# Kernel tuning notes

Measured on AMD Instinct MI355X. Metric: run time of the kernel, lower is better.

The kernel has to match this reference:

```python
import jax, jax.numpy as jnp
import numpy as np

N = 100000      # nodes
E = 1600000     # edges
IN = 128        # in_channels
HID = 32        # hidden_channels
HEADS = 4
G = 256         # number of graphs in the batch
NEG_SLOPE = 0.2


def setup_inputs() -> dict:
    key = jax.random.key(0)
    ks = jax.random.split(key, 20)
    s = 0.1
    d = {
        'x': jax.random.normal(ks[0], (N, IN), jnp.float32),
        'edge_index': jax.random.randint(ks[1], (2, E), 0, N, dtype=jnp.int64),
        'batch': jnp.sort(jax.random.randint(ks[2], (N,), 0, G, dtype=jnp.int64)),
        # conv1: IN -> HID per head, HEADS heads, concat
        'W1': jax.random.normal(ks[3], (IN, HEADS * HID), jnp.float32) * s,
        'a_src1': jax.random.normal(ks[4], (HEADS, HID), jnp.float32) * s,
        'a_dst1': jax.random.normal(ks[5], (HEADS, HID), jnp.float32) * s,
        'b1': jnp.zeros((HEADS * HID,), jnp.float32),
        # conv2: HEADS*HID -> HID per head, HEADS heads, concat
        'W2': jax.random.normal(ks[6], (HEADS * HID, HEADS * HID), jnp.float32) * s,
        'a_src2': jax.random.normal(ks[7], (HEADS, HID), jnp.float32) * s,
        'a_dst2': jax.random.normal(ks[8], (HEADS, HID), jnp.float32) * s,
        'b2': jnp.zeros((HEADS * HID,), jnp.float32),
        # conv3: HEADS*HID -> HID, 1 head, no concat (mean over heads is identity)
        'W3': jax.random.normal(ks[9], (HEADS * HID, HID), jnp.float32) * s,
        'a_src3': jax.random.normal(ks[10], (1, HID), jnp.float32) * s,
        'a_dst3': jax.random.normal(ks[11], (1, HID), jnp.float32) * s,
        'b3': jnp.zeros((HID,), jnp.float32),
        # final readout
        'fc_w': jax.random.normal(ks[12], (HID, 1), jnp.float32) * s,
        'fc_b': jnp.zeros((1,), jnp.float32),
    }
    return d


def _gat_layer(x, src, dst, W, a_s, a_d, b, concat):
    """One PyG-style GATConv: edge attention logits, per-destination softmax, scatter-aggregate."""
    n = x.shape[0]
    H, C = a_s.shape
    h = (x @ W).reshape(n, H, C)                       # [N, H, C]
    asrc = (h * a_s).sum(-1)                           # [N, H]
    adst = (h * a_d).sum(-1)                           # [N, H]
    e = jax.nn.leaky_relu(asrc[src] + adst[dst], NEG_SLOPE)   # [Etot, H]
    m = jax.ops.segment_max(e, dst, num_segments=n)    # per-dst max (self-loops guarantee non-empty)
    ex = jnp.exp(e - m[dst])
    den = jax.ops.segment_sum(ex, dst, num_segments=n)
    alpha = ex / (den[dst] + 1e-16)                    # segment softmax, [Etot, H]
    out = jax.ops.segment_sum(alpha[:, :, None] * h[src], dst, num_segments=n)  # [N, H, C]
    if concat:
        return out.reshape(n, H * C) + b
    return out.mean(axis=1) + b


def reference(x, edge_index, batch, W1, a_src1, a_dst1, b1, W2, a_src2, a_dst2, b2,
              W3, a_src3, a_dst3, b3, fc_w, fc_b):
    n = x.shape[0]
    loops = jnp.arange(n, dtype=edge_index.dtype)      # GATConv adds self-loops by default
    src = jnp.concatenate([edge_index[0], loops])
    dst = jnp.concatenate([edge_index[1], loops])

    h = jax.nn.elu(_gat_layer(x, src, dst, W1, a_src1, a_dst1, b1, True))
    h = jax.nn.elu(_gat_layer(h, src, dst, W2, a_src2, a_dst2, b2, True))
    h = jax.nn.elu(_gat_layer(h, src, dst, W3, a_src3, a_dst3, b3, False))

    counts = jax.ops.segment_sum(jnp.ones((n,), h.dtype), batch, num_segments=G)
    pooled = jax.ops.segment_sum(h, batch, num_segments=G) / jnp.maximum(counts, 1.0)[:, None]
    # dropout p=0.5 is identity in eval mode
    return pooled @ fc_w + fc_b                        # [G, 1]
```

## Files before the change

### kernel.cpp

```cpp
#include <hip/hip_runtime.h>
#include <hip/hip_bf16.h>
#include <math.h>

#define NEG_SLOPE 0.2f
#define CHUNK 6144

typedef short bf16x8 __attribute__((ext_vector_type(8)));
typedef float f32x4  __attribute__((ext_vector_type(4)));

__device__ __forceinline__ float leaky(float x){ return x > 0.f ? x : NEG_SLOPE*x; }
__device__ __forceinline__ float elu(float x){ return x > 0.f ? x : expm1f(x); }

__device__ __forceinline__ ushort f2bf(float f){
  uint u = __float_as_uint(f);
  u += 0x7fffu + ((u >> 16) & 1u);
  return (ushort)(u >> 16);
}
__device__ __forceinline__ uint pk2(float lo, float hi){
  return (uint)f2bf(lo) | ((uint)f2bf(hi) << 16);
}
__device__ __forceinline__ float2 bfpair(uint v){
  return make_float2(__uint_as_float(v << 16), __uint_as_float(v & 0xffff0000u));
}

__global__ __launch_bounds__(256) void k_histA(const int* __restrict__ ei, int E,
                                               int* __restrict__ bucketCount){
  __shared__ int hist[512];
  for (int b = threadIdx.x; b < 512; b += 256) hist[b] = 0;
  __syncthreads();
  int base = blockIdx.x * 2048;
  int cnt = min(2048, E - base);
  for (int i = threadIdx.x; i < cnt; i += 256)
    atomicAdd(&hist[ei[E + base + i] >> 8], 1);
  __syncthreads();
  for (int b = threadIdx.x; b < 512; b += 256)
    if (hist[b]) atomicAdd(&bucketCount[b], hist[b]);
}

__global__ __launch_bounds__(256) void k_scanB(const int* __restrict__ bucketCount, int NB,
                        int* __restrict__ bucketBase, int* __restrict__ gcursor, int E){
  __shared__ int s[512];
  for (int b = threadIdx.x; b < 512; b += 256)
    s[b] = (b < NB) ? bucketCount[b] : 0;
  __syncthreads();
  if (threadIdx.x == 0){
    int run = 0;
    for (int b = 0; b < NB; b++){ int v = s[b]; s[b] = run; run += v; }
  }
  __syncthreads();
  for (int b = threadIdx.x; b < NB; b += 256){
    bucketBase[b] = s[b]; gcursor[b] = s[b];
  }
  if (threadIdx.x == 0) bucketBase[NB] = E;
}

__global__ __launch_bounds__(256) void k_scatA(const int* __restrict__ ei, int E, int NB,
                         int* __restrict__ gcursor, uint* __restrict__ tmp){
  __shared__ uint stageS[CHUNK];
  __shared__ uint stageD[CHUNK];
  __shared__ int hist[512], pre[512], cur[512], gbase[512];
  __shared__ int scanArr[256];
  int tid = threadIdx.x;
  int base = blockIdx.x * CHUNK;
  int cnt = min(CHUNK, E - base);
  for (int b = tid; b < 512; b += 256) hist[b] = 0;
  __syncthreads();
  for (int i = tid; i < cnt; i += 256)
    atomicAdd(&hist[ei[E + base + i] >> 8], 1);
  __syncthreads();
  int a0 = hist[2*tid], a1 = hist[2*tid+1];
  scanArr[tid] = a0 + a1;
  __syncthreads();
  for (int st = 1; st < 256; st <<= 1){
    int v = (tid >= st) ? scanArr[tid - st] : 0;
    __syncthreads();
    scanArr[tid] += v;
    __syncthreads();
  }
  int eb = tid ? scanArr[tid-1] : 0;
  pre[2*tid] = eb;        cur[2*tid] = eb;
  pre[2*tid+1] = eb + a0; cur[2*tid+1] = eb + a0;
  if (2*tid < NB && a0 > 0)   gbase[2*tid]   = atomicAdd(&gcursor[2*tid],   a0);
  if (2*tid+1 < NB && a1 > 0) gbase[2*tid+1] = atomicAdd(&gcursor[2*tid+1], a1);
  __syncthreads();
  for (int i = tid; i < cnt; i += 256){
    int s = ei[base + i];
    int d = ei[E + base + i];
    int lpos = atomicAdd(&cur[d >> 8], 1);
    stageS[lpos] = (uint)s; stageD[lpos] = (uint)d;
  }
  __syncthreads();
  for (int i = tid; i < cnt; i += 256){
    uint d = stageD[i];
    int b = d >> 8;
    tmp[gbase[b] + (i - pre[b])] = (stageS[i] << 8) | (d & 255u);
  }
}

__global__ __launch_bounds__(256) void k_csr(const uint* __restrict__ tmp,
                      const int* __restrict__ bucketBase,
                      int N, int NB, int* __restrict__ offsets, int* __restrict__ csr,
                      int* __restrict__ edst){
  int b = blockIdx.x;
  int nodeBase = b << 8;
  int nNodes = min(256, N - nodeBase);
  int eBeg = bucketBase[b], eEnd = bucketBase[b+1];
  __shared__ int deg[256], cur[256];
  int tid = threadIdx.x;
  deg[tid] = 0;
  __syncthreads();
  for (int e = eBeg + tid; e < eEnd; e += 256)
    atomicAdd(&deg[tmp[e] & 255u], 1);
  __syncthreads();
  cur[tid] = deg[tid];
  __syncthreads();
  for (int st = 1; st < 256; st <<= 1){
    int w = (tid >= st) ? cur[tid - st] : 0;
    __syncthreads();
    cur[tid] += w;
    __syncthreads();
  }
  int excl = tid ? cur[tid-1] : 0;
  __syncthreads();
  cur[tid] = excl;
  if (tid < nNodes) offsets[nodeBase + tid] = eBeg + excl;
  if (b == NB-1 && tid == 0) offsets[N] = eEnd;
  __syncthreads();
  for (int e = eBeg + tid; e < eEnd; e += 256){
    uint u = tmp[e];
    int lpos = atomicAdd(&cur[u & 255u], 1);
    csr[eBeg + lpos] = (int)(u >> 8);
    edst[eBeg + lpos] = nodeBase + (int)(u & 255u);
  }
}

template<int NT>
__global__ __launch_bounds__(256) void k_wrep(const float* __restrict__ W, ushort* __restrict__ Wf){
  int idx = blockIdx.x*256 + threadIdx.x;
  if (idx >= NT*4*64) return;
  int lane = idx & 63;
  int c = (idx >> 6) & 3;
  int t = idx >> 8;
  int col = t*16 + (lane & 15);
  int k0 = c*32 + (lane >> 4)*8;
  uint4 o;
  const float* p0 = W + (size_t)k0*(NT*16) + col;
  o.x = pk2(p0[0],          p0[NT*16]);
  o.y = pk2(p0[2*NT*16],    p0[3*NT*16]);
  o.z = pk2(p0[4*NT*16],    p0[5*NT*16]);
  o.w = pk2(p0[6*NT*16],    p0[7*NT*16]);
  *(uint4*)(Wf + (size_t)idx*8) = o;
}

template<int NT, bool A_F32>
__global__ __launch_bounds__(256) void k_mgemm(const void* __restrict__ Xv,
                     const ushort* __restrict__ Wf, ushort* __restrict__ Y, int n){
  constexpr int M = NT*16;
  int lane = threadIdx.x & 63;
  int l15 = lane & 15, q = lane >> 4;
  int wgid = blockIdx.x*4 + (threadIdx.x >> 6);
  int nchunks = (n + 15) >> 4;
  int stride = gridDim.x*4;

  bf16x8 bw[NT][4];
  #pragma unroll
  for (int t = 0; t < NT; t++)
    #pragma unroll
    for (int c = 0; c < 4; c++)
      bw[t][c] = *(const bf16x8*)(Wf + (size_t)(((t<<2)+c)*64 + lane)*8);

  int chunk = wgid;
  if (chunk >= nchunks) return;

  bf16x8 aCur[4], aNext[4];
  auto loadA = [&](int ck, bf16x8* a){
    int m = ck*16 + l15;
    if (m >= n) m = n - 1;
    if (A_F32){
      const float* X = (const float*)Xv + (size_t)m*128 + q*8;
      #pragma unroll
      for (int c = 0; c < 4; c++){
        float4 u0 = *(const float4*)(X + c*32);
        float4 u1 = *(const float4*)(X + c*32 + 4);
        uint4 pkd;
        pkd.x = pk2(u0.x, u0.y); pkd.y = pk2(u0.z, u0.w);
        pkd.z = pk2(u1.x, u1.y); pkd.w = pk2(u1.z, u1.w);
        union { uint4 u; bf16x8 v; } cv; cv.u = pkd;
        a[c] = cv.v;
      }
    } else {
      const ushort* X = (const ushort*)Xv + (size_t)m*128 + q*8;
      #pragma unroll
      for (int c = 0; c < 4; c++) a[c] = *(const bf16x8*)(X + c*32);
    }
  };

  loadA(chunk, aCur);
  while (true){
    int nx = chunk + stride;
    if (nx < nchunks) loadA(nx, aNext);
    f32x4 acc[NT];
    #pragma unroll
    for (int t = 0; t < NT; t++) acc[t] = (f32x4){0.f,0.f,0.f,0.f};
    #pragma unroll
    for (int c = 0; c < 4; c++)
      #pragma unroll
      for (int t = 0; t < NT; t++)
        acc[t] = __builtin_amdgcn_mfma_f32_16x16x32_bf16(aCur[c], bw[t][c], acc[t], 0, 0, 0);
    int rowb = chunk*16 + q*4;
    #pragma unroll
    for (int t = 0; t < NT; t++)
      #pragma unroll
      for (int r = 0; r < 4; r++){
        int row = rowb + r;
        if (row < n) Y[(size_t)row*M + t*16 + l15] = f2bf(acc[t][r]);
      }
    if (nx >= nchunks) break;
    chunk = nx;
    #pragma unroll
    for (int c = 0; c < 4; c++) aCur[c] = aNext[c];
  }
}

__global__ __launch_bounds__(256) void k_attn(const ushort* __restrict__ Hb, const float* __restrict__ a_s,
                     const float* __restrict__ a_d, float* __restrict__ asrc, float* __restrict__ adst,
                     int n, int H, int M){
  int idx = blockIdx.x*256 + threadIdx.x;
  if (idx >= n*H) return;
  int node = idx / H, h = idx - node*H;
  const uint4* r4 = (const uint4*)(Hb + (size_t)node*M + h*32);
  const float* as = a_s + h*32;
  const float* ad = a_d + h*32;
  float s1 = 0.f, s2 = 0.f;
  #pragma unroll
  for (int i = 0; i < 4; i++){
    uint4 qv = r4[i];
    uint w[4] = {qv.x, qv.y, qv.z, qv.w};
    #pragma unroll
    for (int j = 0; j < 4; j++){
      float2 f = bfpair(w[j]);
      int c = i*8 + j*2;
      s1 += f.x*as[c] + f.y*as[c+1];
      s2 += f.x*ad[c] + f.y*ad[c+1];
    }
  }
  asrc[idx] = s1; adst[idx] = s2;
}

__global__ __launch_bounds__(256) void k_edgew1(const float* __restrict__ asrc,
                    const float* __restrict__ adst, const int* __restrict__ csr,
                    const int* __restrict__ edst, float* __restrict__ ew, int E){
  int e = blockIdx.x*256 + threadIdx.x;
  if (e >= E) return;
  int s = csr[e], d = edst[e];
  ew[e] = __expf(leaky(asrc[s] + adst[d]));
}

template<bool OUT_BF16>
__global__ __launch_bounds__(256) void k_agg128f(const ushort* __restrict__ Hb,
                    const float* __restrict__ asrc, const float* __restrict__ adst,
                    const int* __restrict__ offsets, const int* __restrict__ csr_src,
                    const float* __restrict__ bias, void* __restrict__ Out, int n){
  __shared__ float lwAll[4][256];
  __shared__ int   lsAll[4][64];
  int wv = threadIdx.x >> 6;
  int lane = threadIdx.x & 63;
  float* lw = lwAll[wv];
  int*   ls = lsAll[wv];
  int node = blockIdx.x*4 + wv;
  if (node >= n) return;
  const int up = lane, ch = up*2, h0 = up >> 4;
  const uint* rows = (const uint*)Hb;
  float4 adv = *(const float4*)(adst + (size_t)node*4);
  float adh = adst[(size_t)node*4 + h0];
  float acc0 = 0.f, acc1 = 0.f, den = 0.f;
  {
    float w = __expf(leaky(asrc[(size_t)node*4 + h0] + adh));
    float2 f = bfpair(rows[(size_t)node*64 + up]);
    den += w; acc0 += w*f.x; acc1 += w*f.y;
  }
  int j0 = offsets[node], end = offsets[node+1];
  for (int base = j0; base < end; base += 64){
    int m = min(64, end - base);
    if (lane < m){
      int s = csr_src[base + lane];
      ls[lane] = s;
      float4 a = *(const float4*)(asrc + (size_t)s*4);
      float4 w4;
      w4.x = __expf(leaky(a.x + adv.x));
      w4.y = __expf(leaky(a.y + adv.y));
      w4.z = __expf(leaky(a.z + adv.z));
      w4.w = __expf(leaky(a.w + adv.w));
      *(float4*)(lw + lane*4) = w4;
    }
    int e = 0;
    for (; e + 8 <= m; e += 8){
      int s0=ls[e+0], s1=ls[e+1], s2=ls[e+2], s3=ls[e+3];
      int s4=ls[e+4], s5=ls[e+5], s6=ls[e+6], s7=ls[e+7];
      float w0=lw[(e+0)*4+h0], w1=lw[(e+1)*4+h0], w2=lw[(e+2)*4+h0], w3=lw[(e+3)*4+h0];
      float w4=lw[(e+4)*4+h0], w5=lw[(e+5)*4+h0], w6=lw[(e+6)*4+h0], w7=lw[(e+7)*4+h0];
      uint r0 = rows[(size_t)s0*64 + up];
      uint r1 = rows[(size_t)s1*64 + up];
      uint r2 = rows[(size_t)s2*64 + up];
      uint r3 = rows[(size_t)s3*64 + up];
      uint r4 = rows[(size_t)s4*64 + up];
      uint r5 = rows[(size_t)s5*64 + up];
      uint r6 = rows[(size_t)s6*64 + up];
      uint r7 = rows[(size_t)s7*64 + up];
      float2 f0=bfpair(r0), f1=bfpair(r1), f2=bfpair(r2), f3=bfpair(r3);
      float2 f4=bfpair(r4), f5=bfpair(r5), f6=bfpair(r6), f7=bfpair(r7);
      den  += ((w0+w1)+(w2+w3)) + ((w4+w5)+(w6+w7));
      acc0 += (w0*f0.x + w1*f1.x + w2*f2.x + w3*f3.x)
            + (w4*f4.x + w5*f5.x + w6*f6.x + w7*f7.x);
      acc1 += (w0*f0.y + w1*f1.y + w2*f2.y + w3*f3.y)
            + (w4*f4.y + w5*f5.y + w6*f6.y + w7*f7.y);
    }
    for (; e < m; e++){
      int s = ls[e];
      float w = lw[e*4 + h0];
      float2 f = bfpair(rows[(size_t)s*64 + up]);
      den += w; acc0 += w*f.x; acc1 += w*f.y;
    }
  }
  float inv = 1.f/(den + 1e-16f);
  float ox = elu(acc0*inv + bias[ch]);
  float oy = elu(acc1*inv + bias[ch+1]);
  if (OUT_BF16){
    ((uint*)Out)[(size_t)node*64 + up] = pk2(ox, oy);
  } else {
    *(float2*)((float*)Out + (size_t)node*128 + ch) = make_float2(ox, oy);
  }
}

__global__ __launch_bounds__(256) void k_agg32(const ushort* __restrict__ Hb,
                    const float* __restrict__ asrc, const float* __restrict__ adst,
                    const float* __restrict__ ew,
                    const int* __restrict__ offsets, const int* __restrict__ csr_src,
                    const float* __restrict__ bias, float* __restrict__ Out, int n){
  constexpr int PAIRS = 16;
  int gid = blockIdx.x*256 + threadIdx.x;
  int wave = gid >> 6;
  int lane = threadIdx.x & 63;
  int node = wave*4 + (lane >> 4);
  int up = lane & 15;
  if (node >= n) return;
  const int ch = up*2;
  const uint* rows = (const uint*)Hb;
  float acc0 = 0.f, acc1 = 0.f, den = 0.f;
  {
    float w = __expf(leaky(asrc[node] + adst[node]));
    float2 f = bfpair(rows[(size_t)node*PAIRS + up]);
    den += w; acc0 += w*f.x; acc1 += w*f.y;
  }
  int j = offsets[node], end = offsets[node+1];
  for (; j + 4 <= end; j += 4){
    int s0 = csr_src[j], s1 = csr_src[j+1], s2 = csr_src[j+2], s3 = csr_src[j+3];
    float w0 = ew[j+0], w1 = ew[j+1], w2 = ew[j+2], w3 = ew[j+3];
    uint r0 = rows[(size_t)s0*PAIRS + up];
    uint r1 = rows[(size_t)s1*PAIRS + up];
    uint r2 = rows[(size_t)s2*PAIRS + up];
    uint r3 = rows[(size_t)s3*PAIRS + up];
    float2 f0 = bfpair(r0), f1 = bfpair(r1), f2 = bfpair(r2), f3 = bfpair(r3);
    den  += (w0 + w1) + (w2 + w3);
    acc0 += w0*f0.x + w1*f1.x + w2*f2.x + w3*f3.x;
    acc1 += w0*f0.y + w1*f1.y + w2*f2.y + w3*f3.y;
  }
  for (; j < end; j++){
    int s = csr_src[j];
    float w = ew[j];
    float2 f = bfpair(rows[(size_t)s*PAIRS + up]);
    den += w; acc0 += w*f.x; acc1 += w*f.y;
  }
  float inv = 1.f/(den + 1e-16f);
  float2 o;
  o.x = elu(acc0*inv + bias[ch]);
  o.y = elu(acc1*inv + bias[ch+1]);
  *(float2*)(Out + (size_t)node*32 + ch) = o;
}

__global__ __launch_bounds__(256) void k_bounds(const int* __restrict__ batch, int n, int G,
                                                int* __restrict__ gstart){
  int i = blockIdx.x*256 + threadIdx.x;
  if (i >= n) return;
  int b = batch[i];
  int bp = (i > 0) ? batch[i-1] : -1;
  for (int g = bp + 1; g <= b; g++) gstart[g] = i;
  if (i == n-1){
    for (int g = b + 1; g <= G; g++) gstart[g] = n;
  }
}

__global__ __launch_bounds__(256) void k_pool2(const float* __restrict__ H3,
                     const int* __restrict__ gstart, const float* __restrict__ fcw,
                     const float* __restrict__ fcb, float* __restrict__ out, int G){
  int g = blockIdx.x;
  int s0 = gstart[g], s1 = gstart[g+1];
  int tid = threadIdx.x;
  int c = tid & 31, r = tid >> 5;
  float sum = 0.f;
  for (int i = s0 + r; i < s1; i += 8)
    sum += H3[(size_t)i*32 + c];
  __shared__ float sh[8][32];
  sh[r][c] = sum;
  __syncthreads();
  if (tid < 32){
    float t = 0.f;
    #pragma unroll
    for (int k = 0; k < 8; k++) t += sh[k][tid];
    t *= fcw[tid];
    #pragma unroll
    for (int off = 16; off; off >>= 1) t += __shfl_down(t, off, 32);
    if (tid == 0){
      float cnt = (float)(s1 - s0); if (cnt < 1.f) cnt = 1.f;
      out[g] = t/cnt + fcb[0];
    }
  }
}

extern "C" void kernel_launch(void* const* d_in, const int* in_sizes, int n_in,
                              void* d_out, int out_size, void* d_ws, size_t ws_size,
                              hipStream_t stream){
  const float* x    = (const float*)d_in[0];
  const int*   ei   = (const int*)d_in[1];
  const int*   batch= (const int*)d_in[2];
  const float* W1   = (const float*)d_in[3];
  const float* as1  = (const float*)d_in[4];
  const float* ad1  = (const float*)d_in[5];
  const float* b1   = (const float*)d_in[6];
  const float* W2   = (const float*)d_in[7];
  const float* as2  = (const float*)d_in[8];
  const float* ad2  = (const float*)d_in[9];
  const float* b2   = (const float*)d_in[10];
  const float* W3   = (const float*)d_in[11];
  const float* as3  = (const float*)d_in[12];
  const float* ad3  = (const float*)d_in[13];
  const float* b3   = (const float*)d_in[14];
  const float* fcw  = (const float*)d_in[15];
  const float* fcb  = (const float*)d_in[16];
  float* out = (float*)d_out;

  const int N = in_sizes[0] / 128;
  const int E = in_sizes[1] / 2;
  const int G = out_size;
  const int NB = (N + 255) >> 8;

  char* p = (char*)d_ws;
  auto alloc = [&](size_t bytes) -> void* {
    void* r = (void*)p;
    p += (bytes + 255) & ~(size_t)255;
    return r;
  };
  ushort* bufH   = (ushort*)alloc((size_t)N*128*sizeof(ushort));
  ushort* aggB   = (ushort*)alloc((size_t)N*128*sizeof(ushort));
  float*  bufA32 = (float*)alloc((size_t)N*32*sizeof(float));
  float*  asrc   = (float*)alloc((size_t)N*4*sizeof(float));
  float*  adst   = (float*)alloc((size_t)N*4*sizeof(float));
  float*  ew     = (float*)alloc((size_t)E*sizeof(float));
  int*    offsets= (int*)alloc((size_t)(N+1)*sizeof(int));
  int*    csr    = (int*)alloc((size_t)E*sizeof(int));
  int*    edst   = (int*)alloc((size_t)E*sizeof(int));
  uint*   tmp    = (uint*)alloc((size_t)E*sizeof(uint));
  int*    bCount = (int*)alloc(512*sizeof(int));
  int*    bBase  = (int*)alloc(520*sizeof(int));
  int*    gcursor= (int*)alloc(512*sizeof(int));
  int*    gstart = (int*)alloc((size_t)(G+1)*sizeof(int));
  ushort* Wf1    = (ushort*)alloc(8*4*64*8*sizeof(ushort));
  ushort* Wf2    = (ushort*)alloc(8*4*64*8*sizeof(ushort));
  ushort* Wf3    = (ushort*)alloc(2*4*64*8*sizeof(ushort));

  hipMemsetAsync(bCount, 0, 512*sizeof(int), stream);

  k_wrep<8><<<8, 256, 0, stream>>>(W1, Wf1);
  k_wrep<8><<<8, 256, 0, stream>>>(W2, Wf2);
  k_wrep<2><<<2, 256, 0, stream>>>(W3, Wf3);

  k_histA<<<(E+2047)/2048, 256, 0, stream>>>(ei, E, bCount);
  k_scanB<<<1, 256, 0, stream>>>(bCount, NB, bBase, gcursor, E);
  k_scatA<<<(E+CHUNK-1)/CHUNK, 256, 0, stream>>>(ei, E, NB, gcursor, tmp);
  k_csr<<<NB, 256, 0, stream>>>(tmp, bBase, N, NB, offsets, csr, edst);
  k_bounds<<<(N+255)/256, 256, 0, stream>>>(batch, N, G, gstart);

  const int GB = 512;
  const int NWB = (N + 3)/4;
  k_mgemm<8, true ><<<GB, 256, 0, stream>>>(x, Wf1, bufH, N);
  k_attn<<<(N*4+255)/256, 256, 0, stream>>>(bufH, as1, ad1, asrc, adst, N, 4, 128);
  k_agg128f<true><<<NWB, 256, 0, stream>>>(bufH, asrc, adst, offsets, csr, b1, aggB, N);
  k_mgemm<8, false><<<GB, 256, 0, stream>>>(aggB, Wf2, bufH, N);
  k_attn<<<(N*4+255)/256, 256, 0, stream>>>(bufH, as2, ad2, asrc, adst, N, 4, 128);
  k_agg128f<true><<<NWB, 256, 0, stream>>>(bufH, asrc, adst, offsets, csr, b2, aggB, N);
  k_mgemm<2, false><<<GB, 256, 0, stream>>>(aggB, Wf3, bufH, N);
  k_attn<<<(N+255)/256, 256, 0, stream>>>(bufH, as3, ad3, asrc, adst, N, 1, 32);
  k_edgew1<<<(E+255)/256, 256, 0, stream>>>(asrc, adst, csr, edst, ew, E);
  int waves3 = (N + 3)/4;
  k_agg32<<<(waves3*64 + 255)/256, 256, 0, stream>>>(bufH, asrc, adst, ew, offsets, csr, b3, bufA32, N);
  k_pool2<<<G, 256, 0, stream>>>(bufA32, gstart, fcw, fcb, out, G);
}
```

Baseline: 481.4 us.

## Fuse layer-3 edge weights into aggregation and split wave across edge pairs

Drops the separate per-edge weight kernel and the edst array, so layer 3 computes attention weights inside the aggregation through a per-node LDS staging buffer. The 128-wide aggregation now has each half-wave handle alternating edges, with each lane loading 8 bytes (4 channels) per row, and the halves are combined with a cross-half shuffle. This removes the edst write in CSR build and the E-sized ew round trip, and doubles the bytes per load in the gather. The cost is extra shuffles, padding edges that use the node itself with zero weight, and half the lanes sitting idle in the epilogue.

```diff
diff --git a/kernel.cpp b/kernel.cpp
--- a/kernel.cpp
+++ b/kernel.cpp
@@ -99,8 +99,7 @@
 
 __global__ __launch_bounds__(256) void k_csr(const uint* __restrict__ tmp,
                       const int* __restrict__ bucketBase,
-                      int N, int NB, int* __restrict__ offsets, int* __restrict__ csr,
-                      int* __restrict__ edst){
+                      int N, int NB, int* __restrict__ offsets, int* __restrict__ csr){
   int b = blockIdx.x;
   int nodeBase = b << 8;
   int nNodes = min(256, N - nodeBase);
@@ -130,7 +129,6 @@
     uint u = tmp[e];
     int lpos = atomicAdd(&cur[u & 255u], 1);
     csr[eBeg + lpos] = (int)(u >> 8);
-    edst[eBeg + lpos] = nodeBase + (int)(u & 255u);
   }
 }
 
@@ -247,15 +245,6 @@
   asrc[idx] = s1; adst[idx] = s2;
 }
 
-__global__ __launch_bounds__(256) void k_edgew1(const float* __restrict__ asrc,
-                    const float* __restrict__ adst, const int* __restrict__ csr,
-                    const int* __restrict__ edst, float* __restrict__ ew, int E){
-  int e = blockIdx.x*256 + threadIdx.x;
-  if (e >= E) return;
-  int s = csr[e], d = edst[e];
-  ew[e] = __expf(leaky(asrc[s] + adst[d]));
-}
-
 template<bool OUT_BF16>
 __global__ __launch_bounds__(256) void k_agg128f(const ushort* __restrict__ Hb,
                     const float* __restrict__ asrc, const float* __restrict__ adst,
@@ -269,15 +258,18 @@
   int*   ls = lsAll[wv];
   int node = blockIdx.x*4 + wv;
   if (node >= n) return;
-  const int up = lane, ch = up*2, h0 = up >> 4;
+  const int half = lane >> 5;
+  const int lp = lane & 31;
+  const int h0 = lp >> 3;
   const uint* rows = (const uint*)Hb;
   float4 adv = *(const float4*)(adst + (size_t)node*4);
-  float adh = adst[(size_t)node*4 + h0];
-  float acc0 = 0.f, acc1 = 0.f, den = 0.f;
+  float adh = (h0==0)?adv.x:(h0==1)?adv.y:(h0==2)?adv.z:adv.w;
+  float acc0=0.f, acc1=0.f, acc2=0.f, acc3=0.f, den=0.f;
   {
-    float w = __expf(leaky(asrc[(size_t)node*4 + h0] + adh));
-    float2 f = bfpair(rows[(size_t)node*64 + up]);
-    den += w; acc0 += w*f.x; acc1 += w*f.y;
+    float w = (half == 0) ? __expf(leaky(asrc[(size_t)node*4 + h0] + adh)) : 0.f;
+    uint2 r = *(const uint2*)(rows + (size_t)node*64 + lp*2);
+    float2 fa = bfpair(r.x), fb = bfpair(r.y);
+    den += w; acc0 += w*fa.x; acc1 += w*fa.y; acc2 += w*fb.x; acc3 += w*fb.y;
   }
   int j0 = offsets[node], end = offsets[node+1];
   for (int base = j0; base < end; base += 64){
@@ -293,85 +285,108 @@
       w4.w = __expf(leaky(a.w + adv.w));
       *(float4*)(lw + lane*4) = w4;
     }
+    if (lane == m){
+      ls[m < 64 ? m : 0] = node;
+      if (m < 64) *(float4*)(lw + m*4) = make_float4(0.f,0.f,0.f,0.f);
+    }
+    int mp = (m + 1) & ~1;
     int e = 0;
-    for (; e + 8 <= m; e += 8){
-      int s0=ls[e+0], s1=ls[e+1], s2=ls[e+2], s3=ls[e+3];
-      int s4=ls[e+4], s5=ls[e+5], s6=ls[e+6], s7=ls[e+7];
-      float w0=lw[(e+0)*4+h0], w1=lw[(e+1)*4+h0], w2=lw[(e+2)*4+h0], w3=lw[(e+3)*4+h0];
-      float w4=lw[(e+4)*4+h0], w5=lw[(e+5)*4+h0], w6=lw[(e+6)*4+h0], w7=lw[(e+7)*4+h0];
-      uint r0 = rows[(size_t)s0*64 + up];
-      uint r1 = rows[(size_t)s1*64 + up];
-      uint r2 = rows[(size_t)s2*64 + up];
-      uint r3 = rows[(size_t)s3*64 + up];
-      uint r4 = rows[(size_t)s4*64 + up];
-      uint r5 = rows[(size_t)s5*64 + up];
-      uint r6 = rows[(size_t)s6*64 + up];
-      uint r7 = rows[(size_t)s7*64 + up];
-      float2 f0=bfpair(r0), f1=bfpair(r1), f2=bfpair(r2), f3=bfpair(r3);
-      float2 f4=bfpair(r4), f5=bfpair(r5), f6=bfpair(r6), f7=bfpair(r7);
-      den  += ((w0+w1)+(w2+w3)) + ((w4+w5)+(w6+w7));
-      acc0 += (w0*f0.x + w1*f1.x + w2*f2.x + w3*f3.x)
-            + (w4*f4.x + w5*f5.x + w6*f6.x + w7*f7.x);
-      acc1 += (w0*f0.y + w1*f1.y + w2*f2.y + w3*f3.y)
-            + (w4*f4.y + w5*f5.y + w6*f6.y + w7*f7.y);
-    }
-    for (; e < m; e++){
-      int s = ls[e];
-      float w = lw[e*4 + h0];
-      float2 f = bfpair(rows[(size_t)s*64 + up]);
-      den += w; acc0 += w*f.x; acc1 += w*f.y;
-    }
-  }
-  float inv = 1.f/(den + 1e-16f);
-  float ox = elu(acc0*inv + bias[ch]);
-  float oy = elu(acc1*inv + bias[ch+1]);
-  if (OUT_BF16){
-    ((uint*)Out)[(size_t)node*64 + up] = pk2(ox, oy);
-  } else {
-    *(float2*)((float*)Out + (size_t)node*128 + ch) = make_float2(ox, oy);
+    for (; e + 8 <= mp; e += 8){
+      int e0 = e+half, e1 = e+2+half, e2 = e+4+half, e3 = e+6+half;
+      int s0 = ls[e0], s1 = ls[e1], s2 = ls[e2], s3 = ls[e3];
+      float w0 = lw[e0*4+h0], w1 = lw[e1*4+h0], w2 = lw[e2*4+h0], w3 = lw[e3*4+h0];
+      uint2 r0 = *(const uint2*)(rows + (size_t)s0*64 + lp*2);
+      uint2 r1 = *(const uint2*)(rows + (size_t)s1*64 + lp*2);
+      uint2 r2 = *(const uint2*)(rows + (size_t)s2*64 + lp*2);
+      uint2 r3 = *(const uint2*)(rows + (size_t)s3*64 + lp*2);
+      float2 a0 = bfpair(r0.x), b0 = bfpair(r0.y);
+      float2 a1 = bfpair(r1.x), b1 = bfpair(r1.y);
+      float2 a2 = bfpair(r2.x), b2 = bfpair(r2.y);
+      float2 a3 = bfpair(r3.x), b3 = bfpair(r3.y);
+      den  += (w0 + w1) + (w2 + w3);
+      acc0 += (w0*a0.x + w1*a1.x) + (w2*a2.x + w3*a3.x);
+      acc1 += (w0*a0.y + w1*a1.y) + (w2*a2.y + w3*a3.y);
+      acc2 += (w0*b0.x + w1*b1.x) + (w2*b2.x + w3*b3.x);
+      acc3 += (w0*b0.y + w1*b1.y) + (w2*b2.y + w3*b3.y);
+    }
+    for (; e < mp; e += 2){
+      int e0 = e + half;
+      int s0 = ls[e0];
+      float w0 = lw[e0*4+h0];
+      uint2 r0 = *(const uint2*)(rows + (size_t)s0*64 + lp*2);
+      float2 a0 = bfpair(r0.x), b0 = bfpair(r0.y);
+      den += w0; acc0 += w0*a0.x; acc1 += w0*a0.y; acc2 += w0*b0.x; acc3 += w0*b0.y;
+    }
+  }
+  den  += __shfl_xor(den, 32);
+  acc0 += __shfl_xor(acc0, 32);
+  acc1 += __shfl_xor(acc1, 32);
+  acc2 += __shfl_xor(acc2, 32);
+  acc3 += __shfl_xor(acc3, 32);
+  if (half == 0){
+    float inv = 1.f/(den + 1e-16f);
+    int ch = lp*4;
+    float4 bv = *(const float4*)(bias + ch);
+    float o0 = elu(acc0*inv + bv.x);
+    float o1 = elu(acc1*inv + bv.y);
+    float o2 = elu(acc2*inv + bv.z);
+    float o3 = elu(acc3*inv + bv.w);
+    if (OUT_BF16){
+      uint2 o; o.x = pk2(o0, o1); o.y = pk2(o2, o3);
+      *(uint2*)((uint*)Out + (size_t)node*64 + lp*2) = o;
+    } else {
+      *(float4*)((float*)Out + (size_t)node*128 + ch) = make_float4(o0, o1, o2, o3);
+    }
   }
 }
 
 __global__ __launch_bounds__(256) void k_agg32(const ushort* __restrict__ Hb,
                     const float* __restrict__ asrc, const float* __restrict__ adst,
-                    const float* __restrict__ ew,
                     const int* __restrict__ offsets, const int* __restrict__ csr_src,
                     const float* __restrict__ bias, float* __restrict__ Out, int n){
-  constexpr int PAIRS = 16;
-  int gid = blockIdx.x*256 + threadIdx.x;
-  int wave = gid >> 6;
+  __shared__ int   lsAll[4][4][16];
+  __shared__ float lwAll[4][4][16];
+  int wv = threadIdx.x >> 6;
   int lane = threadIdx.x & 63;
-  int node = wave*4 + (lane >> 4);
-  int up = lane & 15;
+  int g = lane >> 4, i = lane & 15;
+  int node = (blockIdx.x*4 + wv)*4 + g;
   if (node >= n) return;
-  const int ch = up*2;
+  int* ls = lsAll[wv][g];
+  float* lw = lwAll[wv][g];
   const uint* rows = (const uint*)Hb;
+  float adn = adst[node];
   float acc0 = 0.f, acc1 = 0.f, den = 0.f;
   {
-    float w = __expf(leaky(asrc[node] + adst[node]));
-    float2 f = bfpair(rows[(size_t)node*PAIRS + up]);
+    float w = __expf(leaky(asrc[node] + adn));
+    float2 f = bfpair(rows[(size_t)node*16 + i]);
     den += w; acc0 += w*f.x; acc1 += w*f.y;
   }
-  int j = offsets[node], end = offsets[node+1];
-  for (; j + 4 <= end; j += 4){
-    int s0 = csr_src[j], s1 = csr_src[j+1], s2 = csr_src[j+2], s3 = csr_src[j+3];
-    float w0 = ew[j+0], w1 = ew[j+1], w2 = ew[j+2], w3 = ew[j+3];
-    uint r0 = rows[(size_t)s0*PAIRS + up];
-    uint r1 = rows[(size_t)s1*PAIRS + up];
-    uint r2 = rows[(size_t)s2*PAIRS + up];
-    uint r3 = rows[(size_t)s3*PAIRS + up];
-    float2 f0 = bfpair(r0), f1 = bfpair(r1), f2 = bfpair(r2), f3 = bfpair(r3);
-    den  += (w0 + w1) + (w2 + w3);
-    acc0 += w0*f0.x + w1*f1.x + w2*f2.x + w3*f3.x;
-    acc1 += w0*f0.y + w1*f1.y + w2*f2.y + w3*f3.y;
-  }
-  for (; j < end; j++){
-    int s = csr_src[j];
-    float w = ew[j];
-    float2 f = bfpair(rows[(size_t)s*PAIRS + up]);
-    den += w; acc0 += w*f.x; acc1 += w*f.y;
+  int j0 = offsets[node], end = offsets[node+1];
+  for (int base = j0; base < end; base += 16){
+    int m = min(16, end - base);
+    {
+      int idx = base + i;
+      bool v = idx < end;
+      int s = v ? csr_src[idx] : node;
+      ls[i] = s;
+      lw[i] = v ? __expf(leaky(asrc[s] + adn)) : 0.f;
+    }
+    int mR = (m + 3) & ~3;
+    for (int e = 0; e < mR; e += 4){
+      int s0 = ls[e], s1 = ls[e+1], s2 = ls[e+2], s3 = ls[e+3];
+      float w0 = lw[e], w1 = lw[e+1], w2 = lw[e+2], w3 = lw[e+3];
+      uint r0 = rows[(size_t)s0*16 + i];
+      uint r1 = rows[(size_t)s1*16 + i];
+      uint r2 = rows[(size_t)s2*16 + i];
+      uint r3 = rows[(size_t)s3*16 + i];
+      float2 f0 = bfpair(r0), f1 = bfpair(r1), f2 = bfpair(r2), f3 = bfpair(r3);
+      den  += (w0 + w1) + (w2 + w3);
+      acc0 += w0*f0.x + w1*f1.x + w2*f2.x + w3*f3.x;
+      acc1 += w0*f0.y + w1*f1.y + w2*f2.y + w3*f3.y;
+    }
   }
   float inv = 1.f/(den + 1e-16f);
+  int ch = i*2;
   float2 o;
   o.x = elu(acc0*inv + bias[ch]);
   o.y = elu(acc1*inv + bias[ch+1]);
@@ -455,10 +470,8 @@
   float*  bufA32 = (float*)alloc((size_t)N*32*sizeof(float));
   float*  asrc   = (float*)alloc((size_t)N*4*sizeof(float));
   float*  adst   = (float*)alloc((size_t)N*4*sizeof(float));
-  float*  ew     = (float*)alloc((size_t)E*sizeof(float));
   int*    offsets= (int*)alloc((size_t)(N+1)*sizeof(int));
   int*    csr    = (int*)alloc((size_t)E*sizeof(int));
-  int*    edst   = (int*)alloc((size_t)E*sizeof(int));
   uint*   tmp    = (uint*)alloc((size_t)E*sizeof(uint));
   int*    bCount = (int*)alloc(512*sizeof(int));
   int*    bBase  = (int*)alloc(520*sizeof(int));
@@ -477,11 +490,12 @@
   k_histA<<<(E+2047)/2048, 256, 0, stream>>>(ei, E, bCount);
   k_scanB<<<1, 256, 0, stream>>>(bCount, NB, bBase, gcursor, E);
   k_scatA<<<(E+CHUNK-1)/CHUNK, 256, 0, stream>>>(ei, E, NB, gcursor, tmp);
-  k_csr<<<NB, 256, 0, stream>>>(tmp, bBase, N, NB, offsets, csr, edst);
+  k_csr<<<NB, 256, 0, stream>>>(tmp, bBase, N, NB, offsets, csr);
   k_bounds<<<(N+255)/256, 256, 0, stream>>>(batch, N, G, gstart);
 
   const int GB = 512;
   const int NWB = (N + 3)/4;
+  const int NWB32 = (N + 15)/16;
   k_mgemm<8, true ><<<GB, 256, 0, stream>>>(x, Wf1, bufH, N);
   k_attn<<<(N*4+255)/256, 256, 0, stream>>>(bufH, as1, ad1, asrc, adst, N, 4, 128);
   k_agg128f<true><<<NWB, 256, 0, stream>>>(bufH, asrc, adst, offsets, csr, b1, aggB, N);
@@ -490,8 +504,6 @@
   k_agg128f<true><<<NWB, 256, 0, stream>>>(bufH, asrc, adst, offsets, csr, b2, aggB, N);
   k_mgemm<2, false><<<GB, 256, 0, stream>>>(aggB, Wf3, bufH, N);
   k_attn<<<(N+255)/256, 256, 0, stream>>>(bufH, as3, ad3, asrc, adst, N, 1, 32);
-  k_edgew1<<<(E+255)/256, 256, 0, stream>>>(asrc, adst, csr, edst, ew, E);
-  int waves3 = (N + 3)/4;
-  k_agg32<<<(waves3*64 + 255)/256, 256, 0, stream>>>(bufH, asrc, adst, ew, offsets, csr, b3, bufA32, N);
+  k_agg32<<<NWB32, 256, 0, stream>>>(bufH, asrc, adst, offsets, csr, b3, bufA32, N);
   k_pool2<<<G, 256, 0, stream>>>(bufA32, gstart, fcw, fcb, out, G);
 }
```

Measured after the change: 500.3 us. +3.9%, slower.

## Fuse layer-3 edge weight computation into aggregation and drop edst array

Applied to the files above, without the earlier changes.

Removes the separate edge-weight kernel and the per-edge destination array. The layer-3 aggregation now computes attention weights cooperatively per 16-edge chunk in shared memory, with each of the 16 lanes of a node group handling one edge. This saves an E-sized write and read of weights and the edst write in CSR construction. The cost is that exp work is duplicated inline and chunks are padded to multiples of 4 with zero-weight entries. A small tweak also reuses the already-loaded adst float4 in agg128f.

```diff
diff --git a/kernel.cpp b/kernel.cpp
--- a/kernel.cpp
+++ b/kernel.cpp
@@ -99,8 +99,7 @@
 
 __global__ __launch_bounds__(256) void k_csr(const uint* __restrict__ tmp,
                       const int* __restrict__ bucketBase,
-                      int N, int NB, int* __restrict__ offsets, int* __restrict__ csr,
-                      int* __restrict__ edst){
+                      int N, int NB, int* __restrict__ offsets, int* __restrict__ csr){
   int b = blockIdx.x;
   int nodeBase = b << 8;
   int nNodes = min(256, N - nodeBase);
@@ -130,7 +129,6 @@
     uint u = tmp[e];
     int lpos = atomicAdd(&cur[u & 255u], 1);
     csr[eBeg + lpos] = (int)(u >> 8);
-    edst[eBeg + lpos] = nodeBase + (int)(u & 255u);
   }
 }
 
@@ -247,15 +245,6 @@
   asrc[idx] = s1; adst[idx] = s2;
 }
 
-__global__ __launch_bounds__(256) void k_edgew1(const float* __restrict__ asrc,
-                    const float* __restrict__ adst, const int* __restrict__ csr,
-                    const int* __restrict__ edst, float* __restrict__ ew, int E){
-  int e = blockIdx.x*256 + threadIdx.x;
-  if (e >= E) return;
-  int s = csr[e], d = edst[e];
-  ew[e] = __expf(leaky(asrc[s] + adst[d]));
-}
-
 template<bool OUT_BF16>
 __global__ __launch_bounds__(256) void k_agg128f(const ushort* __restrict__ Hb,
                     const float* __restrict__ asrc, const float* __restrict__ adst,
@@ -272,7 +261,7 @@
   const int up = lane, ch = up*2, h0 = up >> 4;
   const uint* rows = (const uint*)Hb;
   float4 adv = *(const float4*)(adst + (size_t)node*4);
-  float adh = adst[(size_t)node*4 + h0];
+  float adh = (h0==0)?adv.x:(h0==1)?adv.y:(h0==2)?adv.z:adv.w;
   float acc0 = 0.f, acc1 = 0.f, den = 0.f;
   {
     float w = __expf(leaky(asrc[(size_t)node*4 + h0] + adh));
@@ -334,44 +323,51 @@
 
 __global__ __launch_bounds__(256) void k_agg32(const ushort* __restrict__ Hb,
                     const float* __restrict__ asrc, const float* __restrict__ adst,
-                    const float* __restrict__ ew,
                     const int* __restrict__ offsets, const int* __restrict__ csr_src,
                     const float* __restrict__ bias, float* __restrict__ Out, int n){
-  constexpr int PAIRS = 16;
-  int gid = blockIdx.x*256 + threadIdx.x;
-  int wave = gid >> 6;
+  __shared__ int   lsAll[4][4][16];
+  __shared__ float lwAll[4][4][16];
+  int wv = threadIdx.x >> 6;
   int lane = threadIdx.x & 63;
-  int node = wave*4 + (lane >> 4);
-  int up = lane & 15;
+  int g = lane >> 4, i = lane & 15;
+  int node = (blockIdx.x*4 + wv)*4 + g;
   if (node >= n) return;
-  const int ch = up*2;
+  int* ls = lsAll[wv][g];
+  float* lw = lwAll[wv][g];
   const uint* rows = (const uint*)Hb;
+  float adn = adst[node];
   float acc0 = 0.f, acc1 = 0.f, den = 0.f;
   {
-    float w = __expf(leaky(asrc[node] + adst[node]));
-    float2 f = bfpair(rows[(size_t)node*PAIRS + up]);
+    float w = __expf(leaky(asrc[node] + adn));
+    float2 f = bfpair(rows[(size_t)node*16 + i]);
     den += w; acc0 += w*f.x; acc1 += w*f.y;
   }
-  int j = offsets[node], end = offsets[node+1];
-  for (; j + 4 <= end; j += 4){
-    int s0 = csr_src[j], s1 = csr_src[j+1], s2 = csr_src[j+2], s3 = csr_src[j+3];
-    float w0 = ew[j+0], w1 = ew[j+1], w2 = ew[j+2], w3 = ew[j+3];
-    uint r0 = rows[(size_t)s0*PAIRS + up];
-    uint r1 = rows[(size_t)s1*PAIRS + up];
-    uint r2 = rows[(size_t)s2*PAIRS + up];
-    uint r3 = rows[(size_t)s3*PAIRS + up];
-    float2 f0 = bfpair(r0), f1 = bfpair(r1), f2 = bfpair(r2), f3 = bfpair(r3);
-    den  += (w0 + w1) + (w2 + w3);
-    acc0 += w0*f0.x + w1*f1.x + w2*f2.x + w3*f3.x;
-    acc1 += w0*f0.y + w1*f1.y + w2*f2.y + w3*f3.y;
-  }
-  for (; j < end; j++){
-    int s = csr_src[j];
-    float w = ew[j];
-    float2 f = bfpair(rows[(size_t)s*PAIRS + up]);
-    den += w; acc0 += w*f.x; acc1 += w*f.y;
+  int j0 = offsets[node], end = offsets[node+1];
+  for (int base = j0; base < end; base += 16){
+    int m = min(16, end - base);
+    {
+      int idx = base + i;
+      bool v = idx < end;
+      int s = v ? csr_src[idx] : node;
+      ls[i] = s;
+      lw[i] = v ? __expf(leaky(asrc[s] + adn)) : 0.f;
+    }
+    int mR = (m + 3) & ~3;
+    for (int e = 0; e < mR; e += 4){
+      int s0 = ls[e], s1 = ls[e+1], s2 = ls[e+2], s3 = ls[e+3];
+      float w0 = lw[e], w1 = lw[e+1], w2 = lw[e+2], w3 = lw[e+3];
+      uint r0 = rows[(size_t)s0*16 + i];
+      uint r1 = rows[(size_t)s1*16 + i];
+      uint r2 = rows[(size_t)s2*16 + i];
+      uint r3 = rows[(size_t)s3*16 + i];
+      float2 f0 = bfpair(r0), f1 = bfpair(r1), f2 = bfpair(r2), f3 = bfpair(r3);
+      den  += (w0 + w1) + (w2 + w3);
+      acc0 += w0*f0.x + w1*f1.x + w2*f2.x + w3*f3.x;
+      acc1 += w0*f0.y + w1*f1.y + w2*f2.y + w3*f3.y;
+    }
   }
   float inv = 1.f/(den + 1e-16f);
+  int ch = i*2;
   float2 o;
   o.x = elu(acc0*inv + bias[ch]);
   o.y = elu(acc1*inv + bias[ch+1]);
@@ -455,10 +451,8 @@
   float*  bufA32 = (float*)alloc((size_t)N*32*sizeof(float));
   float*  asrc   = (float*)alloc((size_t)N*4*sizeof(float));
   float*  adst   = (float*)alloc((size_t)N*4*sizeof(float));
-  float*  ew     = (float*)alloc((size_t)E*sizeof(float));
   int*    offsets= (int*)alloc((size_t)(N+1)*sizeof(int));
   int*    csr    = (int*)alloc((size_t)E*sizeof(int));
-  int*    edst   = (int*)alloc((size_t)E*sizeof(int));
   uint*   tmp    = (uint*)alloc((size_t)E*sizeof(uint));
   int*    bCount = (int*)alloc(512*sizeof(int));
   int*    bBase  = (int*)alloc(520*sizeof(int));
@@ -477,11 +471,12 @@
   k_histA<<<(E+2047)/2048, 256, 0, stream>>>(ei, E, bCount);
   k_scanB<<<1, 256, 0, stream>>>(bCount, NB, bBase, gcursor, E);
   k_scatA<<<(E+CHUNK-1)/CHUNK, 256, 0, stream>>>(ei, E, NB, gcursor, tmp);
-  k_csr<<<NB, 256, 0, stream>>>(tmp, bBase, N, NB, offsets, csr, edst);
+  k_csr<<<NB, 256, 0, stream>>>(tmp, bBase, N, NB, offsets, csr);
   k_bounds<<<(N+255)/256, 256, 0, stream>>>(batch, N, G, gstart);
 
   const int GB = 512;
   const int NWB = (N + 3)/4;
+  const int NWB32 = (N + 15)/16;
   k_mgemm<8, true ><<<GB, 256, 0, stream>>>(x, Wf1, bufH, N);
   k_attn<<<(N*4+255)/256, 256, 0, stream>>>(bufH, as1, ad1, asrc, adst, N, 4, 128);
   k_agg128f<true><<<NWB, 256, 0, stream>>>(bufH, asrc, adst, offsets, csr, b1, aggB, N);
@@ -490,8 +485,6 @@
   k_agg128f<true><<<NWB, 256, 0, stream>>>(bufH, asrc, adst, offsets, csr, b2, aggB, N);
   k_mgemm<2, false><<<GB, 256, 0, stream>>>(aggB, Wf3, bufH, N);
   k_attn<<<(N+255)/256, 256, 0, stream>>>(bufH, as3, ad3, asrc, adst, N, 1, 32);
-  k_edgew1<<<(E+255)/256, 256, 0, stream>>>(asrc, adst, csr, edst, ew, E);
-  int waves3 = (N + 3)/4;
-  k_agg32<<<(waves3*64 + 255)/256, 256, 0, stream>>>(bufH, asrc, adst, ew, offsets, csr, b3, bufA32, N);
+  k_agg32<<<NWB32, 256, 0, stream>>>(bufH, asrc, adst, offsets, csr, b3, bufA32, N);
   k_pool2<<<G, 256, 0, stream>>>(bufA32, gstart, fcw, fcb, out, G);
 }
```

Result: faster. 460.9 us (-4.3%).
